# Performance work log

Measured on AMD Instinct MI355X. Metric: run time of the kernel, lower is better.

Reference implementation:

```python
import jax, jax.numpy as jnp
import numpy as np

K = 3
CINS = [1, 16, 32, 48, 64]
COUTS = [16, 32, 48, 64, 80]
POOL = [True, True, True, False, False]


def _bilinear(x, py, px):
    # x: [B,C,H,W]; py,px: [B,K2,H,W] float sample coords. Zero padding outside.
    B, C, H, W = x.shape
    y0 = jnp.floor(py)
    x0 = jnp.floor(px)
    wy = (py - y0)[:, None]  # [B,1,K2,H,W]
    wx = (px - x0)[:, None]
    y0i = y0.astype(jnp.int32)
    x0i = x0.astype(jnp.int32)
    xf = x.reshape(B, C, H * W)

    def gather(yi, xi):
        valid = (yi >= 0) & (yi < H) & (xi >= 0) & (xi < W)
        yc = jnp.clip(yi, 0, H - 1)
        xc = jnp.clip(xi, 0, W - 1)
        flat = (yc * W + xc).reshape(B, 1, -1)
        v = jnp.take_along_axis(xf, jnp.broadcast_to(flat, (B, C, flat.shape[-1])), axis=2)
        v = v.reshape(B, C, *yi.shape[1:])
        return v * valid[:, None].astype(x.dtype)

    v00 = gather(y0i, x0i)
    v01 = gather(y0i, x0i + 1)
    v10 = gather(y0i + 1, x0i)
    v11 = gather(y0i + 1, x0i + 1)
    return (v00 * (1 - wy) * (1 - wx) + v01 * (1 - wy) * wx
            + v10 * wy * (1 - wx) + v11 * wy * wx)


def _deform_conv(x, woff, boff, w):
    # torchvision DeformConv2d v1: offsets from a regular conv, layout [B, 2*K*K, H, W]
    # with (dy, dx) pairs per kernel tap; stride=1, pad=1, dilation=1.
    B, C, H, W = x.shape
    off = jax.lax.conv_general_dilated(
        x, woff, (1, 1), ((1, 1), (1, 1)),
        dimension_numbers=('NCHW', 'OIHW', 'NCHW')) + boff[None, :, None, None]
    off = off.reshape(B, K * K, 2, H, W)
    ky, kx = jnp.meshgrid(jnp.arange(K), jnp.arange(K), indexing='ij')
    # sample position: p = (h - pad + ky + dy, w - pad + kx + dx)
    py = off[:, :, 0] + (jnp.arange(H, dtype=x.dtype)[None, None, :, None] - 1.0) \
        + ky.reshape(-1).astype(x.dtype)[None, :, None, None]
    px = off[:, :, 1] + (jnp.arange(W, dtype=x.dtype)[None, None, None, :] - 1.0) \
        + kx.reshape(-1).astype(x.dtype)[None, :, None, None]
    samp = _bilinear(x, py, px)  # [B,C,K2,H,W]
    return jnp.einsum('bckhw,ock->bohw', samp, w.reshape(w.shape[0], C, K * K))


def _bn_lrelu(x, g, b):
    # BatchNorm2d training-mode forward (batch stats, biased var, eps=1e-5) + LeakyReLU(0.01)
    m = x.mean((0, 2, 3), keepdims=True)
    v = ((x - m) ** 2).mean((0, 2, 3), keepdims=True)
    y = g[None, :, None, None] * (x - m) * jax.lax.rsqrt(v + 1e-5) + b[None, :, None, None]
    return jnp.where(y > 0, y, 0.01 * y)


def _pool(x):
    return jax.lax.reduce_window(x, -jnp.inf, jax.lax.max, (1, 1, 2, 2), (1, 1, 2, 2), 'VALID')


def _forward(x, params):
    for i, pool in enumerate(POOL):
        woff, boff, w, g, b = params[i]
        x = _bn_lrelu(_deform_conv(x, woff, boff, w), g, b)
        if pool:
            x = _pool(x)
    return x


def setup_inputs() -> dict:
    key = jax.random.key(0)
    ks = jax.random.split(key, 8)
    inp = {"x": jax.random.normal(ks[0], (8, 1, 128, 1024), jnp.float32)}
    for i, (ci, co) in enumerate(zip(CINS, COUTS)):
        k1, k2, k3, k4, k5 = jax.random.split(ks[i + 1], 5)
        inp[f"woff{i}"] = jax.random.normal(k1, (2 * K * K, ci, K, K), jnp.float32) * 0.05
        inp[f"boff{i}"] = jax.random.normal(k2, (2 * K * K,), jnp.float32) * 0.01
        inp[f"w{i}"] = jax.random.normal(k3, (co, ci, K, K), jnp.float32) / np.float32(np.sqrt(ci * K * K))
        inp[f"g{i}"] = jnp.ones((co,), jnp.float32) + 0.1 * jax.random.normal(k4, (co,), jnp.float32)
        inp[f"b{i}"] = 0.1 * jax.random.normal(k5, (co,), jnp.float32)
    return inp


def reference(x, woff0, boff0, w0, g0, b0, woff1, boff1, w1, g1, b1,
              woff2, boff2, w2, g2, b2, woff3, boff3, w3, g3, b3,
              woff4, boff4, w4, g4, b4):
    params = [(woff0, boff0, w0, g0, b0), (woff1, boff1, w1, g1, b1),
              (woff2, boff2, w2, g2, b2), (woff3, boff3, w3, g3, b3),
              (woff4, boff4, w4, g4, b4)]
    return _forward(x, params)
```

## Files before the change

### kernel.cpp

```cpp
#include <hip/hip_runtime.h>
#include <math.h>

#define TPB 256


#define OWM0 0
#define OWM1 144
#define OWM2 4752
#define OWM3 18576
#define OWM4 46224
#define OWO0 92304
#define OWO1 92484
#define OWO2 95940
#define OWO3 102852
#define OWO4 113220
#define PACK_FLOATS 131072

struct PackSrc { const float* p[10]; };

__global__ void pack_weights(PackSrc s, float* __restrict__ dst) {
  int seg = blockIdx.y;
  int idx = blockIdx.x * TPB + threadIdx.x;
  int CI, CO, ow;
  if (seg < 5) {
    if (seg == 0)      { CI = 1;  CO = 16; ow = OWM0; }
    else if (seg == 1) { CI = 16; CO = 32; ow = OWM1; }
    else if (seg == 2) { CI = 32; CO = 48; ow = OWM2; }
    else if (seg == 3) { CI = 48; CO = 64; ow = OWM3; }
    else               { CI = 64; CO = 80; ow = OWM4; }
    int n = 9 * CI * CO;
    if (idx >= n) return;
    int o = idx % CO, rest = idx / CO;
    int c = rest % CI, k = rest / CI;
    dst[ow + idx] = s.p[seg][((size_t)o * CI + c) * 9 + k];
  } else if (seg == 5) {
    if (idx >= 180) return;
    int j = idx % 20, t = idx / 20;
    dst[OWO0 + idx] = (j < 18) ? s.p[5][j * 9 + t] : 0.f;
  } else {
    if (seg == 6)      { CI = 16; ow = OWO1; }
    else if (seg == 7) { CI = 32; ow = OWO2; }
    else if (seg == 8) { CI = 48; ow = OWO3; }
    else               { CI = 64; ow = OWO4; }
    int n = 3 * CI * 9 * 8;
    if (idx >= n) return;
    int u = idx % 8, r = idx / 8;
    int t = r % 9, c = (r / 9) % CI, jg = r / (9 * CI);
    dst[ow + idx] = (u < 6) ? s.p[seg][((size_t)(jg * 6 + u) * CI + c) * 9 + t] : 0.f;
  }
}

__device__ __forceinline__ int xcd_swz(int bid, int nwg) {
  return (bid & 7) * (nwg >> 3) + (bid >> 3);
}

__global__ __launch_bounds__(TPB) void dfc_fused0(
    const float* __restrict__ x, const float* __restrict__ woP,
    const float* __restrict__ boff, const float* __restrict__ wmP,
    float* __restrict__ out, int B, int H, int W) {
  const int idx = xcd_swz(blockIdx.x, gridDim.x) * TPB + threadIdx.x;
  const int HW = H * W;
  const int w = idx % W;
  const int h = (idx / W) % H;
  const int b = idx / HW;
  const float* xp = x + (size_t)b * HW;

  float xv[9];
#pragma unroll
  for (int t = 0; t < 9; t++) {
    int yy = h - 1 + t / 3, xx = w - 1 + t % 3;
    xv[t] = (yy >= 0 && yy < H && xx >= 0 && xx < W) ? xp[yy * W + xx] : 0.f;
  }

  float offv[18];
#pragma unroll
  for (int j = 0; j < 18; j++) offv[j] = boff[j];
#pragma unroll
  for (int t = 0; t < 9; t++) {
    const float* wr = &woP[t * 20];
#pragma unroll
    for (int j = 0; j < 18; j++) offv[j] = fmaf(xv[t], wr[j], offv[j]);
  }

  float acc[16];
#pragma unroll
  for (int o = 0; o < 16; o++) acc[o] = 0.f;

#pragma unroll
  for (int k = 0; k < 9; k++) {
    float py = (float)(h - 1 + k / 3) + offv[2 * k];
    float px = (float)(w - 1 + k % 3) + offv[2 * k + 1];
    float fy = floorf(py), fx = floorf(px);
    float wy = py - fy, wx = px - fx;
    int y0 = (int)fy, x0 = (int)fx;
    int y1 = y0 + 1, x1 = x0 + 1;
    bool vy0 = (y0 >= 0) & (y0 < H), vy1 = (y1 >= 0) & (y1 < H);
    bool vx0 = (x0 >= 0) & (x0 < W), vx1 = (x1 >= 0) & (x1 < W);
    int yc0 = min(max(y0, 0), H - 1), yc1 = min(max(y1, 0), H - 1);
    int xc0 = min(max(x0, 0), W - 1), xc1 = min(max(x1, 0), W - 1);
    float w00 = (vy0 && vx0) ? (1.f - wy) * (1.f - wx) : 0.f;
    float w01 = (vy0 && vx1) ? (1.f - wy) * wx : 0.f;
    float w10 = (vy1 && vx0) ? wy * (1.f - wx) : 0.f;
    float w11 = (vy1 && vx1) ? wy * wx : 0.f;
    float sv = xp[yc0 * W + xc0] * w00 + xp[yc0 * W + xc1] * w01
             + xp[yc1 * W + xc0] * w10 + xp[yc1 * W + xc1] * w11;
    const float* wr = &wmP[k * 16];
#pragma unroll
    for (int o = 0; o < 16; o++) acc[o] = fmaf(sv, wr[o], acc[o]);
  }

  float* op = out + (size_t)b * 16 * HW + h * W + w;
#pragma unroll
  for (int o = 0; o < 16; o++) op[(size_t)o * HW] = acc[o];
}

template<int CI, int TPBK>
__global__ __launch_bounds__(TPBK) void off_conv(
    const float* __restrict__ x, const float* __restrict__ wP,
    const float* __restrict__ boff, float* __restrict__ off,
    int B, int H, int W) {
  const int HW = H * W;
  const int npb = HW / TPBK;
  const int bid = xcd_swz(blockIdx.x, gridDim.x);
  const int pxb = bid % npb;
  const int jg = (bid / npb) % 3;
  const int b = bid / (3 * npb);
  const int px = pxb * TPBK + threadIdx.x;
  const int w = px % W, h = px / W;
  const float* xb = x + (size_t)b * HW * CI;
  const float* wj = wP + (size_t)jg * CI * 9 * 8;

  float acc[6];
#pragma unroll
  for (int u = 0; u < 6; u++) acc[u] = boff[jg * 6 + u];

#pragma unroll 1
  for (int t = 0; t < 9; t++) {
    int yy = h - 1 + t / 3, xx = w - 1 + t % 3;
    bool vld = (yy >= 0 && yy < H && xx >= 0 && xx < W);
    int a = vld ? (yy * W + xx) : 0;
    const float* xp = xb + (size_t)a * CI;
    const float* wt = wj + t * 8;
#pragma unroll 4
    for (int cg = 0; cg < CI / 4; cg++) {
      float4 v = *(const float4*)(xp + cg * 4);
      float s0 = vld ? v.x : 0.f;
      float s1 = vld ? v.y : 0.f;
      float s2 = vld ? v.z : 0.f;
      float s3 = vld ? v.w : 0.f;
      const float* w0 = wt + (size_t)cg * 4 * 72;
#pragma unroll
      for (int u = 0; u < 6; u++) {
        float a0 = fmaf(s0, w0[u], acc[u]);
        float a1 = fmaf(s1, w0[72 + u], a0);
        float a2 = fmaf(s2, w0[144 + u], a1);
        acc[u] = fmaf(s3, w0[216 + u], a2);
      }
    }
  }
#pragma unroll
  for (int u = 0; u < 6; u++)
    off[((size_t)b * 18 + jg * 6 + u) * HW + px] = acc[u];
}

template<int CI, int CO, int OGC, int TPBK>
__global__ __launch_bounds__(TPBK) void dfc_og(
    const float* __restrict__ x, const float* __restrict__ off,
    const float* __restrict__ wP, float* __restrict__ out,
    int B, int H, int W) {
  constexpr int COG = CO / OGC;
  const int HW = H * W;
  const int npb = HW / TPBK;
  const int bid = xcd_swz(blockIdx.x, gridDim.x);
  const int og = bid % OGC;
  const int pxb = (bid / OGC) % npb;
  const int b = bid / (OGC * npb);
  const int px = pxb * TPBK + threadIdx.x;
  const int w = px % W, h = px / W;
  const float* xb = x + (size_t)b * HW * CI;

  float offv[18];
  const float* ob = off + (size_t)b * 18 * HW + px;
#pragma unroll
  for (int j = 0; j < 18; j++) offv[j] = ob[(size_t)j * HW];

  float acc[COG];
#pragma unroll
  for (int o = 0; o < COG; o++) acc[o] = 0.f;

#pragma unroll
  for (int k = 0; k < 9; k++) {
    float py = (float)(h - 1 + k / 3) + offv[2 * k];
    float pxx = (float)(w - 1 + k % 3) + offv[2 * k + 1];
    float fy = floorf(py), fx = floorf(pxx);
    float wy = py - fy, wx = pxx - fx;
    int y0 = (int)fy, x0 = (int)fx;
    int y1 = y0 + 1, x1 = x0 + 1;
    bool vy0 = (y0 >= 0) & (y0 < H), vy1 = (y1 >= 0) & (y1 < H);
    bool vx0 = (x0 >= 0) & (x0 < W), vx1 = (x1 >= 0) & (x1 < W);
    int yc0 = min(max(y0, 0), H - 1), yc1 = min(max(y1, 0), H - 1);
    int xc0 = min(max(x0, 0), W - 1), xc1 = min(max(x1, 0), W - 1);
    float w00 = (vy0 && vx0) ? (1.f - wy) * (1.f - wx) : 0.f;
    float w01 = (vy0 && vx1) ? (1.f - wy) * wx : 0.f;
    float w10 = (vy1 && vx0) ? wy * (1.f - wx) : 0.f;
    float w11 = (vy1 && vx1) ? wy * wx : 0.f;
    const float* p00 = xb + (size_t)(yc0 * W + xc0) * CI;
    const float* p01 = xb + (size_t)(yc0 * W + xc1) * CI;
    const float* p10 = xb + (size_t)(yc1 * W + xc0) * CI;
    const float* p11 = xb + (size_t)(yc1 * W + xc1) * CI;
#pragma unroll 2
    for (int cg = 0; cg < CI / 4; cg++) {
      float4 v00 = *(const float4*)(p00 + cg * 4);
      float4 v01 = *(const float4*)(p01 + cg * 4);
      float4 v10 = *(const float4*)(p10 + cg * 4);
      float4 v11 = *(const float4*)(p11 + cg * 4);
      float s0 = v00.x * w00 + v01.x * w01 + v10.x * w10 + v11.x * w11;
      float s1 = v00.y * w00 + v01.y * w01 + v10.y * w10 + v11.y * w11;
      float s2 = v00.z * w00 + v01.z * w01 + v10.z * w10 + v11.z * w11;
      float s3 = v00.w * w00 + v01.w * w01 + v10.w * w10 + v11.w * w11;
      const float* wr = wP + (size_t)(k * CI + cg * 4) * CO + og * COG;
#pragma unroll
      for (int o = 0; o < COG; o++) {
        float a0 = fmaf(s0, wr[o], acc[o]);
        float a1 = fmaf(s1, wr[CO + o], a0);
        float a2 = fmaf(s2, wr[2 * CO + o], a1);
        acc[o] = fmaf(s3, wr[3 * CO + o], a2);
      }
    }
  }

  float* op = out + ((size_t)b * CO + og * COG) * HW + px;
#pragma unroll
  for (int o = 0; o < COG; o++) op[(size_t)o * HW] = acc[o];
}

__global__ void bn_stats_kernel(const float* __restrict__ y,
                                double* __restrict__ st,
                                int B, int C, int HW, int NB) {
  int c = blockIdx.x / NB;
  int sl = blockIdx.x % NB;
  int tid = threadIdx.x;
  double s = 0.0, s2 = 0.0;
  int HW4 = HW >> 2;
  for (int b = 0; b < B; b++) {
    const float4* p = (const float4*)(y + ((size_t)b * C + c) * HW);
    for (int i = sl * TPB + tid; i < HW4; i += NB * TPB) {
      float4 v = p[i];
      s += (double)v.x + (double)v.y + (double)v.z + (double)v.w;
      s2 += (double)v.x * v.x + (double)v.y * v.y
          + (double)v.z * v.z + (double)v.w * v.w;
    }
  }
  __shared__ double rs[TPB], rq[TPB];
  rs[tid] = s;
  rq[tid] = s2;
  __syncthreads();
  for (int o = TPB / 2; o > 0; o >>= 1) {
    if (tid < o) { rs[tid] += rs[tid + o]; rq[tid] += rq[tid + o]; }
    __syncthreads();
  }
  if (tid == 0) {
    atomicAdd(&st[2 * c], rs[0]);
    atomicAdd(&st[2 * c + 1], rq[0]);
  }
}

__global__ void bn_finalize_kernel(const double* __restrict__ st,
                                   const float* __restrict__ g,
                                   const float* __restrict__ bb,
                                   float* __restrict__ ss, int C, int N) {
  int c = threadIdx.x;
  if (c >= C) return;
  double mean = st[2 * c] / N;
  double var = st[2 * c + 1] / N - mean * mean;
  float inv = (float)(1.0 / sqrt(var + 1e-5));
  float sc = g[c] * inv;
  ss[c] = sc;
  ss[C + c] = bb[c] - (float)mean * sc;
}

__global__ void bn_apply_kernel(const float* __restrict__ y,
                                const float* __restrict__ ss,
                                float* __restrict__ out, int C, int HW, int n) {
  int i = blockIdx.x * TPB + threadIdx.x;
  if (i >= n) return;
  int c = (i / HW) % C;
  float v = fmaf(y[i], ss[c], ss[C + c]);
  out[i] = v > 0.f ? v : 0.01f * v;
}

__global__ void bn_apply_nhwc_kernel(const float* __restrict__ y,
                                     const float* __restrict__ ss,
                                     float* __restrict__ out,
                                     int C, int H, int W, int n) {
  int i = blockIdx.x * TPB + threadIdx.x;
  if (i >= n) return;
  int c = i % C;
  int pix = i / C;
  int w = pix % W;
  int h = (pix / W) % H;
  int b = pix / (W * H);
  float v = fmaf(y[(((size_t)b * C + c) * H + h) * W + w], ss[c], ss[C + c]);
  out[i] = v > 0.f ? v : 0.01f * v;
}

__global__ void bn_apply_pool_nhwc_kernel(const float* __restrict__ y,
                                          const float* __restrict__ ss,
                                          float* __restrict__ out,
                                          int C, int H, int W, int n) {
  int i = blockIdx.x * TPB + threadIdx.x;
  if (i >= n) return;
  int Wp = W >> 1, Hp = H >> 1;
  int c = i % C;
  int pw = (i / C) % Wp;
  int ph = (i / C / Wp) % Hp;
  int b = i / (C * Wp * Hp);
  const float* yp = y + (((size_t)b * C + c) * H + 2 * ph) * W + 2 * pw;
  float sc = ss[c], sh = ss[C + c];
  float v0 = fmaf(yp[0], sc, sh);     v0 = v0 > 0.f ? v0 : 0.01f * v0;
  float v1 = fmaf(yp[1], sc, sh);     v1 = v1 > 0.f ? v1 : 0.01f * v1;
  float v2 = fmaf(yp[W], sc, sh);     v2 = v2 > 0.f ? v2 : 0.01f * v2;
  float v3 = fmaf(yp[W + 1], sc, sh); v3 = v3 > 0.f ? v3 : 0.01f * v3;
  out[i] = fmaxf(fmaxf(v0, v1), fmaxf(v2, v3));
}

extern "C" void kernel_launch(void* const* d_in, const int* in_sizes, int n_in,
                              void* d_out, int out_size, void* d_ws, size_t ws_size,
                              hipStream_t stream) {
  const float* x = (const float*)d_in[0];
  const float *woff[5], *boff[5], *wm[5], *g[5], *bb[5];
  for (int i = 0; i < 5; i++) {
    woff[i] = (const float*)d_in[1 + 5 * i + 0];
    boff[i] = (const float*)d_in[1 + 5 * i + 1];
    wm[i]   = (const float*)d_in[1 + 5 * i + 2];
    g[i]    = (const float*)d_in[1 + 5 * i + 3];
    bb[i]   = (const float*)d_in[1 + 5 * i + 4];
  }

  const size_t need =
      (size_t)(16777216 + 4718592 + 4194304 + 2097152 + PACK_FLOATS) * 4 + 6400 + 640;
  if (ws_size < need) return;

  float* conv_buf = (float*)d_ws;
  float* off_buf = conv_buf + 16777216;
  float* xa = off_buf + 4718592;
  float* xb2 = xa + 4194304;
  float* wpk = xb2 + 2097152;
  double* st = (double*)(wpk + PACK_FLOATS);
  float* ss = (float*)(st + 800);

  const int B = 8;

  {
    PackSrc psrc;
    for (int i = 0; i < 5; i++) { psrc.p[i] = wm[i]; psrc.p[5 + i] = woff[i]; }
    pack_weights<<<dim3(180, 10), TPB, 0, stream>>>(psrc, wpk);
    hipMemsetAsync(st, 0, 800 * sizeof(double), stream);
  }

  auto bn_head = [&](const float* ybuf, int C, int H, int W, int NB,
                     const float* gg, const float* bbb, int layer) {
    double* stl = st + 160 * layer;
    bn_stats_kernel<<<C * NB, TPB, 0, stream>>>(ybuf, stl, B, C, H * W, NB);
    bn_finalize_kernel<<<1, TPB, 0, stream>>>(stl, gg, bbb, ss, C, B * H * W);
  };

  {
    const int H = 128, W = 1024;
    dfc_fused0<<<B * H * W / TPB, TPB, 0, stream>>>(
        x, wpk + OWO0, boff[0], wpk + OWM0, conv_buf, B, H, W);
    bn_head(conv_buf, 16, H, W, 32, g[0], bb[0], 0);
    int n = B * 16 * (H / 2) * (W / 2);
    bn_apply_pool_nhwc_kernel<<<n / TPB, TPB, 0, stream>>>(
        conv_buf, ss, xa, 16, H, W, n);
  }
  {
    const int H = 64, W = 512;
    off_conv<16, 256><<<B * 3 * (H * W / 256), 256, 0, stream>>>(
        xa, wpk + OWO1, boff[1], off_buf, B, H, W);
    dfc_og<16, 32, 1, 256><<<B * (H * W / 256), 256, 0, stream>>>(
        xa, off_buf, wpk + OWM1, conv_buf, B, H, W);
    bn_head(conv_buf, 32, H, W, 32, g[1], bb[1], 1);
    int n = B * 32 * (H / 2) * (W / 2);
    bn_apply_pool_nhwc_kernel<<<n / TPB, TPB, 0, stream>>>(
        conv_buf, ss, xb2, 32, H, W, n);
  }
  {
    const int H = 32, W = 256;
    off_conv<32, 256><<<B * 3 * (H * W / 256), 256, 0, stream>>>(
        xb2, wpk + OWO2, boff[2], off_buf, B, H, W);
    dfc_og<32, 48, 2, 256><<<B * (H * W / 256) * 2, 256, 0, stream>>>(
        xb2, off_buf, wpk + OWM2, conv_buf, B, H, W);
    bn_head(conv_buf, 48, H, W, 16, g[2], bb[2], 2);
    int n = B * 48 * (H / 2) * (W / 2);
    bn_apply_pool_nhwc_kernel<<<n / TPB, TPB, 0, stream>>>(
        conv_buf, ss, xa, 48, H, W, n);
  }
  {
    const int H = 16, W = 128;
    off_conv<48, 64><<<B * 3 * (H * W / 64), 64, 0, stream>>>(
        xa, wpk + OWO3, boff[3], off_buf, B, H, W);
    dfc_og<48, 64, 8, 64><<<B * (H * W / 64) * 8, 64, 0, stream>>>(
        xa, off_buf, wpk + OWM3, conv_buf, B, H, W);
    bn_head(conv_buf, 64, H, W, 8, g[3], bb[3], 3);
    int n = B * 64 * H * W;
    bn_apply_nhwc_kernel<<<n / TPB, TPB, 0, stream>>>(
        conv_buf, ss, xb2, 64, H, W, n);
  }
  {
    const int H = 16, W = 128;
    off_conv<64, 64><<<B * 3 * (H * W / 64), 64, 0, stream>>>(
        xb2, wpk + OWO4, boff[4], off_buf, B, H, W);
    dfc_og<64, 80, 10, 64><<<B * (H * W / 64) * 10, 64, 0, stream>>>(
        xb2, off_buf, wpk + OWM4, conv_buf, B, H, W);
    bn_head(conv_buf, 80, H, W, 8, g[4], bb[4], 4);
    int n = B * 80 * H * W;
    bn_apply_kernel<<<n / TPB, TPB, 0, stream>>>(
        conv_buf, ss, (float*)d_out, 80, H * W, n);
  }
}
```

Measured before the change: 582.8 us.

## Share bilinear samples via LDS across output-channel warps in deformable conv layers 2-4

Adds a new deformable-conv kernel that computes the bilinear samples for a 64-pixel tile once per kernel tap, cooperatively across all channel groups, and stores them in shared memory. Each of the four waves then reads those samples and accumulates a distinct slice of output channels. The aim is to remove the redundant gather and interpolation work the old kernel repeated for every output-channel group. The cost is two barriers per tap, extra LDS traffic, and fewer, larger blocks for layers 2 to 4.

```diff
diff --git a/kernel.cpp b/kernel.cpp
--- a/kernel.cpp
+++ b/kernel.cpp
@@ -234,6 +234,100 @@
   for (int o = 0; o < COG; o++) op[(size_t)o * HW] = acc[o];
 }
 
+template<int CI, int CO, int OGB>
+__global__ __launch_bounds__(TPB) void dfc_slds(
+    const float* __restrict__ x, const float* __restrict__ off,
+    const float* __restrict__ wP, float* __restrict__ out,
+    int B, int H, int W) {
+  constexpr int P = 64;
+  constexpr int S = CI / 4;
+  constexpr int COG = CO / (4 * OGB);
+  constexpr int ROWD = P * 4 + 4;
+  constexpr int NT = (P * S) / TPB;
+
+  __shared__ float s_off[18 * P];
+  __shared__ float s_samp[S * ROWD];
+
+  const int HW = H * W;
+  const int npb = HW / P;
+  const int bid = xcd_swz(blockIdx.x, gridDim.x);
+  const int ogb = bid % OGB;
+  const int pxb = (bid / OGB) % npb;
+  const int b = bid / (OGB * npb);
+  const int px0 = pxb * P;
+  const int tid = threadIdx.x;
+  const float* xb = x + (size_t)b * HW * CI;
+
+  for (int t = tid; t < 18 * P; t += TPB) {
+    int j = t / P, p = t % P;
+    s_off[t] = off[((size_t)b * 18 + j) * HW + px0 + p];
+  }
+
+  const int pc = tid & 63;
+  const int wid = tid >> 6;
+  const int ocb = (ogb * 4 + wid) * COG;
+
+  float acc[COG];
+#pragma unroll
+  for (int o = 0; o < COG; o++) acc[o] = 0.f;
+
+#pragma unroll 1
+  for (int k = 0; k < 9; k++) {
+    __syncthreads();
+#pragma unroll 1
+    for (int tt = 0; tt < NT; tt++) {
+      int t = tt * TPB + tid;
+      int s = t % S, p = t / S;
+      int px = px0 + p;
+      int w = px % W, h = px / W;
+      float dy = s_off[(2 * k) * P + p];
+      float dx = s_off[(2 * k + 1) * P + p];
+      float py = (float)(h - 1 + k / 3) + dy;
+      float pxx = (float)(w - 1 + k % 3) + dx;
+      float fy = floorf(py), fx = floorf(pxx);
+      float wy = py - fy, wx = pxx - fx;
+      int y0 = (int)fy, x0 = (int)fx;
+      int y1 = y0 + 1, x1 = x0 + 1;
+      bool vy0 = (y0 >= 0) & (y0 < H), vy1 = (y1 >= 0) & (y1 < H);
+      bool vx0 = (x0 >= 0) & (x0 < W), vx1 = (x1 >= 0) & (x1 < W);
+      int yc0 = min(max(y0, 0), H - 1), yc1 = min(max(y1, 0), H - 1);
+      int xc0 = min(max(x0, 0), W - 1), xc1 = min(max(x1, 0), W - 1);
+      float w00 = (vy0 && vx0) ? (1.f - wy) * (1.f - wx) : 0.f;
+      float w01 = (vy0 && vx1) ? (1.f - wy) * wx : 0.f;
+      float w10 = (vy1 && vx0) ? wy * (1.f - wx) : 0.f;
+      float w11 = (vy1 && vx1) ? wy * wx : 0.f;
+      float4 v00 = *(const float4*)(xb + (size_t)(yc0 * W + xc0) * CI + s * 4);
+      float4 v01 = *(const float4*)(xb + (size_t)(yc0 * W + xc1) * CI + s * 4);
+      float4 v10 = *(const float4*)(xb + (size_t)(yc1 * W + xc0) * CI + s * 4);
+      float4 v11 = *(const float4*)(xb + (size_t)(yc1 * W + xc1) * CI + s * 4);
+      float4 sv;
+      sv.x = v00.x * w00 + v01.x * w01 + v10.x * w10 + v11.x * w11;
+      sv.y = v00.y * w00 + v01.y * w01 + v10.y * w10 + v11.y * w11;
+      sv.z = v00.z * w00 + v01.z * w01 + v10.z * w10 + v11.z * w11;
+      sv.w = v00.w * w00 + v01.w * w01 + v10.w * w10 + v11.w * w11;
+      *(float4*)&s_samp[s * ROWD + p * 4] = sv;
+    }
+    __syncthreads();
+#pragma unroll
+    for (int s = 0; s < S; s++) {
+      float4 sv = *(const float4*)&s_samp[s * ROWD + pc * 4];
+      float sj0 = sv.x, sj1 = sv.y, sj2 = sv.z, sj3 = sv.w;
+      const float* wr = wP + (size_t)(k * CI + s * 4) * CO + ocb;
+#pragma unroll
+      for (int o = 0; o < COG; o++) {
+        float a0 = fmaf(sj0, wr[o], acc[o]);
+        float a1 = fmaf(sj1, wr[CO + o], a0);
+        float a2 = fmaf(sj2, wr[2 * CO + o], a1);
+        acc[o] = fmaf(sj3, wr[3 * CO + o], a2);
+      }
+    }
+  }
+
+  float* op = out + ((size_t)b * CO + ocb) * HW + px0 + pc;
+#pragma unroll
+  for (int o = 0; o < COG; o++) op[(size_t)o * HW] = acc[o];
+}
+
 __global__ void bn_stats_kernel(const float* __restrict__ y,
                                 double* __restrict__ st,
                                 int B, int C, int HW, int NB) {
@@ -389,7 +483,7 @@
     const int H = 32, W = 256;
     off_conv<32, 256><<<B * 3 * (H * W / 256), 256, 0, stream>>>(
         xb2, wpk + OWO2, boff[2], off_buf, B, H, W);
-    dfc_og<32, 48, 2, 256><<<B * (H * W / 256) * 2, 256, 0, stream>>>(
+    dfc_slds<32, 48, 1><<<B * (H * W / 64), TPB, 0, stream>>>(
         xb2, off_buf, wpk + OWM2, conv_buf, B, H, W);
     bn_head(conv_buf, 48, H, W, 16, g[2], bb[2], 2);
     int n = B * 48 * (H / 2) * (W / 2);
@@ -400,7 +494,7 @@
     const int H = 16, W = 128;
     off_conv<48, 64><<<B * 3 * (H * W / 64), 64, 0, stream>>>(
         xa, wpk + OWO3, boff[3], off_buf, B, H, W);
-    dfc_og<48, 64, 8, 64><<<B * (H * W / 64) * 8, 64, 0, stream>>>(
+    dfc_slds<48, 64, 2><<<B * (H * W / 64) * 2, TPB, 0, stream>>>(
         xa, off_buf, wpk + OWM3, conv_buf, B, H, W);
     bn_head(conv_buf, 64, H, W, 8, g[3], bb[3], 3);
     int n = B * 64 * H * W;
@@ -411,7 +505,7 @@
     const int H = 16, W = 128;
     off_conv<64, 64><<<B * 3 * (H * W / 64), 64, 0, stream>>>(
         xb2, wpk + OWO4, boff[4], off_buf, B, H, W);
-    dfc_og<64, 80, 10, 64><<<B * (H * W / 64) * 10, 64, 0, stream>>>(
+    dfc_slds<64, 80, 2><<<B * (H * W / 64) * 2, TPB, 0, stream>>>(
         xb2, off_buf, wpk + OWM4, conv_buf, B, H, W);
     bn_head(conv_buf, 80, H, W, 8, g[4], bb[4], 4);
     int n = B * 80 * H * W;
```

Result: slower. 598.6 us (+2.7%).

## Split deformable conv kernel taps across blocks with partial-sum buffers for small layers

Applied to the files above, without the earlier changes.

For layers 3 and 4 (16x128 spatial), the deformable conv now splits the 9 kernel taps into 3 groups handled by separate blocks. Each group writes a partial output plane, and the BN stats and apply kernels sum the three partials as they read them. The aim is more parallelism on the small late layers, where the grid was too small to fill the GPU. The cost is extra partial-output memory traffic and three reads per element in the BN kernels, and the output-channel grouping is halved to keep the block count balanced.

```diff
diff --git a/kernel.cpp b/kernel.cpp
--- a/kernel.cpp
+++ b/kernel.cpp
@@ -163,35 +163,40 @@
     off[((size_t)b * 18 + jg * 6 + u) * HW + px] = acc[u];
 }
 
-template<int CI, int CO, int OGC, int TPBK>
+template<int CI, int CO, int OGC, int TPBK, int NKG>
 __global__ __launch_bounds__(TPBK) void dfc_og(
     const float* __restrict__ x, const float* __restrict__ off,
     const float* __restrict__ wP, float* __restrict__ out,
     int B, int H, int W) {
   constexpr int COG = CO / OGC;
+  constexpr int KPG = 9 / NKG;
   const int HW = H * W;
   const int npb = HW / TPBK;
   const int bid = xcd_swz(blockIdx.x, gridDim.x);
   const int og = bid % OGC;
-  const int pxb = (bid / OGC) % npb;
-  const int b = bid / (OGC * npb);
+  int r = bid / OGC;
+  const int pxb = r % npb; r /= npb;
+  const int kg = r % NKG;
+  const int b = r / NKG;
   const int px = pxb * TPBK + threadIdx.x;
   const int w = px % W, h = px / W;
   const float* xb = x + (size_t)b * HW * CI;
 
-  float offv[18];
+  float offv[2 * KPG];
   const float* ob = off + (size_t)b * 18 * HW + px;
 #pragma unroll
-  for (int j = 0; j < 18; j++) offv[j] = ob[(size_t)j * HW];
+  for (int j = 0; j < 2 * KPG; j++)
+    offv[j] = ob[(size_t)(kg * 2 * KPG + j) * HW];
 
   float acc[COG];
 #pragma unroll
   for (int o = 0; o < COG; o++) acc[o] = 0.f;
 
 #pragma unroll
-  for (int k = 0; k < 9; k++) {
-    float py = (float)(h - 1 + k / 3) + offv[2 * k];
-    float pxx = (float)(w - 1 + k % 3) + offv[2 * k + 1];
+  for (int kk = 0; kk < KPG; kk++) {
+    const int k = kg * KPG + kk;
+    float py = (float)(h - 1 + k / 3) + offv[2 * kk];
+    float pxx = (float)(w - 1 + k % 3) + offv[2 * kk + 1];
     float fy = floorf(py), fx = floorf(pxx);
     float wy = py - fy, wx = pxx - fx;
     int y0 = (int)fy, x0 = (int)fx;
@@ -229,12 +234,14 @@
     }
   }
 
-  float* op = out + ((size_t)b * CO + og * COG) * HW + px;
+  float* op = out + (size_t)kg * B * CO * HW
+            + ((size_t)b * CO + og * COG) * HW + px;
 #pragma unroll
   for (int o = 0; o < COG; o++) op[(size_t)o * HW] = acc[o];
 }
 
-__global__ void bn_stats_kernel(const float* __restrict__ y,
+template<int NP>
+__global__ void bn_stats_kernel(const float* __restrict__ y, size_t ps,
                                 double* __restrict__ st,
                                 int B, int C, int HW, int NB) {
   int c = blockIdx.x / NB;
@@ -243,9 +250,15 @@
   double s = 0.0, s2 = 0.0;
   int HW4 = HW >> 2;
   for (int b = 0; b < B; b++) {
-    const float4* p = (const float4*)(y + ((size_t)b * C + c) * HW);
+    size_t base = ((size_t)b * C + c) * HW;
     for (int i = sl * TPB + tid; i < HW4; i += NB * TPB) {
-      float4 v = p[i];
+      float4 v = *(const float4*)(y + base + 4 * (size_t)i);
+      if (NP > 1) {
+        float4 v1 = *(const float4*)(y + ps + base + 4 * (size_t)i);
+        float4 v2 = *(const float4*)(y + 2 * ps + base + 4 * (size_t)i);
+        v.x += v1.x + v2.x; v.y += v1.y + v2.y;
+        v.z += v1.z + v2.z; v.w += v1.w + v2.w;
+      }
       s += (double)v.x + (double)v.y + (double)v.z + (double)v.w;
       s2 += (double)v.x * v.x + (double)v.y * v.y
           + (double)v.z * v.z + (double)v.w * v.w;
@@ -279,17 +292,21 @@
   ss[C + c] = bb[c] - (float)mean * sc;
 }
 
-__global__ void bn_apply_kernel(const float* __restrict__ y,
+template<int NP>
+__global__ void bn_apply_kernel(const float* __restrict__ y, size_t ps,
                                 const float* __restrict__ ss,
                                 float* __restrict__ out, int C, int HW, int n) {
   int i = blockIdx.x * TPB + threadIdx.x;
   if (i >= n) return;
+  float yv = y[i];
+  if (NP > 1) yv += y[ps + i] + y[2 * ps + i];
   int c = (i / HW) % C;
-  float v = fmaf(y[i], ss[c], ss[C + c]);
+  float v = fmaf(yv, ss[c], ss[C + c]);
   out[i] = v > 0.f ? v : 0.01f * v;
 }
 
-__global__ void bn_apply_nhwc_kernel(const float* __restrict__ y,
+template<int NP>
+__global__ void bn_apply_nhwc_kernel(const float* __restrict__ y, size_t ps,
                                      const float* __restrict__ ss,
                                      float* __restrict__ out,
                                      int C, int H, int W, int n) {
@@ -300,7 +317,10 @@
   int w = pix % W;
   int h = (pix / W) % H;
   int b = pix / (W * H);
-  float v = fmaf(y[(((size_t)b * C + c) * H + h) * W + w], ss[c], ss[C + c]);
+  size_t a = (((size_t)b * C + c) * H + h) * W + w;
+  float yv = y[a];
+  if (NP > 1) yv += y[ps + a] + y[2 * ps + a];
+  float v = fmaf(yv, ss[c], ss[C + c]);
   out[i] = v > 0.f ? v : 0.01f * v;
 }
 
@@ -358,18 +378,12 @@
     hipMemsetAsync(st, 0, 800 * sizeof(double), stream);
   }
 
-  auto bn_head = [&](const float* ybuf, int C, int H, int W, int NB,
-                     const float* gg, const float* bbb, int layer) {
-    double* stl = st + 160 * layer;
-    bn_stats_kernel<<<C * NB, TPB, 0, stream>>>(ybuf, stl, B, C, H * W, NB);
-    bn_finalize_kernel<<<1, TPB, 0, stream>>>(stl, gg, bbb, ss, C, B * H * W);
-  };
-
   {
     const int H = 128, W = 1024;
     dfc_fused0<<<B * H * W / TPB, TPB, 0, stream>>>(
         x, wpk + OWO0, boff[0], wpk + OWM0, conv_buf, B, H, W);
-    bn_head(conv_buf, 16, H, W, 32, g[0], bb[0], 0);
+    bn_stats_kernel<1><<<16 * 32, TPB, 0, stream>>>(conv_buf, 0, st, B, 16, H * W, 32);
+    bn_finalize_kernel<<<1, TPB, 0, stream>>>(st, g[0], bb[0], ss, 16, B * H * W);
     int n = B * 16 * (H / 2) * (W / 2);
     bn_apply_pool_nhwc_kernel<<<n / TPB, TPB, 0, stream>>>(
         conv_buf, ss, xa, 16, H, W, n);
@@ -378,9 +392,10 @@
     const int H = 64, W = 512;
     off_conv<16, 256><<<B * 3 * (H * W / 256), 256, 0, stream>>>(
         xa, wpk + OWO1, boff[1], off_buf, B, H, W);
-    dfc_og<16, 32, 1, 256><<<B * (H * W / 256), 256, 0, stream>>>(
+    dfc_og<16, 32, 1, 256, 1><<<B * (H * W / 256), 256, 0, stream>>>(
         xa, off_buf, wpk + OWM1, conv_buf, B, H, W);
-    bn_head(conv_buf, 32, H, W, 32, g[1], bb[1], 1);
+    bn_stats_kernel<1><<<32 * 32, TPB, 0, stream>>>(conv_buf, 0, st + 160, B, 32, H * W, 32);
+    bn_finalize_kernel<<<1, TPB, 0, stream>>>(st + 160, g[1], bb[1], ss, 32, B * H * W);
     int n = B * 32 * (H / 2) * (W / 2);
     bn_apply_pool_nhwc_kernel<<<n / TPB, TPB, 0, stream>>>(
         conv_buf, ss, xb2, 32, H, W, n);
@@ -389,33 +404,38 @@
     const int H = 32, W = 256;
     off_conv<32, 256><<<B * 3 * (H * W / 256), 256, 0, stream>>>(
         xb2, wpk + OWO2, boff[2], off_buf, B, H, W);
-    dfc_og<32, 48, 2, 256><<<B * (H * W / 256) * 2, 256, 0, stream>>>(
+    dfc_og<32, 48, 2, 256, 1><<<B * (H * W / 256) * 2, 256, 0, stream>>>(
         xb2, off_buf, wpk + OWM2, conv_buf, B, H, W);
-    bn_head(conv_buf, 48, H, W, 16, g[2], bb[2], 2);
+    bn_stats_kernel<1><<<48 * 16, TPB, 0, stream>>>(conv_buf, 0, st + 320, B, 48, H * W, 16);
+    bn_finalize_kernel<<<1, TPB, 0, stream>>>(st + 320, g[2], bb[2], ss, 48, B * H * W);
     int n = B * 48 * (H / 2) * (W / 2);
     bn_apply_pool_nhwc_kernel<<<n / TPB, TPB, 0, stream>>>(
         conv_buf, ss, xa, 48, H, W, n);
   }
   {
     const int H = 16, W = 128;
+    const size_t ps = (size_t)B * 64 * H * W;
     off_conv<48, 64><<<B * 3 * (H * W / 64), 64, 0, stream>>>(
         xa, wpk + OWO3, boff[3], off_buf, B, H, W);
-    dfc_og<48, 64, 8, 64><<<B * (H * W / 64) * 8, 64, 0, stream>>>(
+    dfc_og<48, 64, 4, 64, 3><<<B * 3 * (H * W / 64) * 4, 64, 0, stream>>>(
         xa, off_buf, wpk + OWM3, conv_buf, B, H, W);
-    bn_head(conv_buf, 64, H, W, 8, g[3], bb[3], 3);
+    bn_stats_kernel<3><<<64 * 8, TPB, 0, stream>>>(conv_buf, ps, st + 480, B, 64, H * W, 8);
+    bn_finalize_kernel<<<1, TPB, 0, stream>>>(st + 480, g[3], bb[3], ss, 64, B * H * W);
     int n = B * 64 * H * W;
-    bn_apply_nhwc_kernel<<<n / TPB, TPB, 0, stream>>>(
-        conv_buf, ss, xb2, 64, H, W, n);
+    bn_apply_nhwc_kernel<3><<<n / TPB, TPB, 0, stream>>>(
+        conv_buf, ps, ss, xb2, 64, H, W, n);
   }
   {
     const int H = 16, W = 128;
+    const size_t ps = (size_t)B * 80 * H * W;
     off_conv<64, 64><<<B * 3 * (H * W / 64), 64, 0, stream>>>(
         xb2, wpk + OWO4, boff[4], off_buf, B, H, W);
-    dfc_og<64, 80, 10, 64><<<B * (H * W / 64) * 10, 64, 0, stream>>>(
+    dfc_og<64, 80, 5, 64, 3><<<B * 3 * (H * W / 64) * 5, 64, 0, stream>>>(
         xb2, off_buf, wpk + OWM4, conv_buf, B, H, W);
-    bn_head(conv_buf, 80, H, W, 8, g[4], bb[4], 4);
+    bn_stats_kernel<3><<<80 * 8, TPB, 0, stream>>>(conv_buf, ps, st + 640, B, 80, H * W, 8);
+    bn_finalize_kernel<<<1, TPB, 0, stream>>>(st + 640, g[4], bb[4], ss, 80, B * H * W);
     int n = B * 80 * H * W;
-    bn_apply_kernel<<<n / TPB, TPB, 0, stream>>>(
-        conv_buf, ss, (float*)d_out, 80, H * W, n);
-  }
-}
+    bn_apply_kernel<3><<<n / TPB, TPB, 0, stream>>>(
+        conv_buf, ps, ss, (float*)d_out, 80, H * W, n);
+  }
+}
```

Result: faster. 570.6 us (-2.1%).
